# Performance work log

Measured on AMD Instinct MI355X. Metric: run time of the kernel, lower is better.

## Reference

```python
import jax, jax.numpy as jnp
import numpy as np


def setup_inputs() -> dict:
    key = jax.random.key(0)
    ks = jax.random.split(key, 8)
    B, S, A = 128, 256, 128   # rows, seq, channels
    H, KD, VD, O = 8, 16, 16, 128
    w_scale = 1.0 / np.sqrt(A)
    return {
        "q_data": jax.random.normal(ks[0], (B, S, A), jnp.float32),
        "bias": jax.random.normal(ks[1], (B, S, S), jnp.float32),
        "nonbatched_bias": jax.random.normal(ks[2], (S, S), jnp.float32),
        "query_w": jax.random.normal(ks[3], (A, H, KD), jnp.float32) * w_scale,
        "key_w": jax.random.normal(ks[4], (A, H, KD), jnp.float32) * w_scale,
        "value_w": jax.random.normal(ks[5], (A, H, VD), jnp.float32) * w_scale,
        "gating_w": jax.random.normal(ks[6], (A, H, VD), jnp.float32) * w_scale,
        "output_w": jax.random.normal(ks[7], (H, VD, O), jnp.float32) * w_scale,
    }


def reference(q_data, bias, nonbatched_bias, query_w, key_w, value_w, gating_w, output_w):
    # Gated multihead self-attention (AlphaFold grid self-attention).
    key_dim = query_w.shape[-1]
    scale = key_dim ** -0.5
    # fused QKV + gate projections from q_data (self-attention: m_data == q_data)
    q = jnp.einsum('bqa,ahc->bqhc', q_data, query_w) * scale
    k = jnp.einsum('bka,ahc->bkhc', q_data, key_w)
    v = jnp.einsum('bka,ahc->bkhc', q_data, value_w)
    # logits [B, H, Q, K] + batched bias + shared nonbatched bias
    logits = (jnp.einsum('bqhc,bkhc->bhqk', q, k)
              + bias[:, None, :, :]
              + nonbatched_bias[None, None, :, :])
    weights = jax.nn.softmax(logits, axis=-1)
    weighted_avg = jnp.einsum('bhqk,bkhc->bqhc', weights, v)
    gate = jax.nn.sigmoid(jnp.einsum('bqa,ahc->bqhc', q_data, gating_w))
    out = jnp.einsum('bqhc,hco->bqo', gate * weighted_avg, output_w)
    return out
```

## Files before the change

kernel.cpp:

```cpp
#include <hip/hip_runtime.h>
#include <math.h>

#define BB 128
#define SS 256
#define AA 128
#define HH 8
#define CC 16
#define HCC 128
#define OO 128

typedef float f32x4 __attribute__((ext_vector_type(4)));
typedef short s16x4 __attribute__((ext_vector_type(4)));
typedef unsigned short u16x4 __attribute__((ext_vector_type(4)));

__device__ __forceinline__ unsigned bf16_rne(float x) {
    union { float f; unsigned u; } v; v.f = x;
    return (v.u + 0x7fffu + ((v.u >> 16) & 1u)) >> 16;
}
__device__ __forceinline__ unsigned pack_bf16(float lo, float hi) {
    return bf16_rne(lo) | (bf16_rne(hi) << 16);
}

__device__ __forceinline__ void mfma16(f32x4& d, s16x4 a, s16x4 b) {
#if __has_builtin(__builtin_amdgcn_mfma_f32_16x16x16bf16_1k)
    d = __builtin_amdgcn_mfma_f32_16x16x16bf16_1k(a, b, d, 0, 0, 0);
#else
    asm("v_mfma_f32_16x16x16_bf16 %0, %1, %2, %0" : "+v"(d) : "v"(a), "v"(b));
#endif
}

__global__ __launch_bounds__(256) void prep_w_kernel(
    const float* __restrict__ wq, const float* __restrict__ wk,
    const float* __restrict__ wv, const float* __restrict__ wg,
    const float* __restrict__ wo, unsigned short* __restrict__ wt16)
{
    const int j = blockIdx.x >> 4;
    const int t = ((blockIdx.x & 15) << 8) + threadIdx.x;
    const float* W = (j == 0) ? wq : (j == 1) ? wk : (j == 2) ? wv
                   : (j == 3) ? wg : wo;
    const int outch = t >> 5;
    const int a0 = (t & 31) * 4;
    u16x4 v;
    #pragma unroll
    for (int u = 0; u < 4; ++u)
        v[u] = (unsigned short)bf16_rne(W[(size_t)(a0 + u) * 128 + outch]);
    char* dst = (char*)wt16 + (size_t)j * 32768 + outch * 256
              + ((a0 * 2) ^ ((outch & 7) << 5));
    *(u16x4*)dst = v;
}

__global__ __launch_bounds__(256) void qkvg_mfma_kernel(
    const float* __restrict__ qdata, const unsigned short* __restrict__ wt16,
    unsigned short* __restrict__ qb, unsigned short* __restrict__ kb,
    unsigned short* __restrict__ vtb, float* __restrict__ g_ws)
{
    __shared__ char wlds[32768];
    const int tid = threadIdx.x;
    const int w = tid >> 6;
    const int lane = tid & 63;
    const int lo = lane & 15, gg = lane >> 4;
    const int sb = blockIdx.x * 64;
    const int s = sb + w * 16 + lo;
    const int b = sb >> 8;
    const int srow = (sb & 255) + w * 16;

    s16x4 qd[8];
    {
        const float* qp = qdata + (size_t)s * AA;
        #pragma unroll
        for (int t = 0; t < 8; ++t) {
            float4 f = *(const float4*)(qp + t * 16 + gg * 4);
            unsigned w0 = pack_bf16(f.x, f.y), w1 = pack_bf16(f.z, f.w);
            s16x4 q; ((unsigned*)&q)[0] = w0; ((unsigned*)&q)[1] = w1;
            qd[t] = q;
        }
    }

    for (int m = 0; m < 4; ++m) {
        __syncthreads();
        {
            const uint4* src = (const uint4*)((const char*)wt16 + m * 32768);
            uint4* dst = (uint4*)wlds;
            #pragma unroll
            for (int i = 0; i < 8; ++i) dst[i * 256 + tid] = src[i * 256 + tid];
        }
        __syncthreads();

        #pragma unroll
        for (int cf = 0; cf < 8; ++cf) {
            s16x4 wf[8];
            #pragma unroll
            for (int t = 0; t < 8; ++t) {
                int boff = (cf * 16 + lo) * 256 + ((t * 32 + gg * 8) ^ ((lo & 7) << 5));
                wf[t] = *(const s16x4*)(wlds + boff);
            }
            f32x4 acc = {0.f, 0.f, 0.f, 0.f};
            if (m == 2) {
                #pragma unroll
                for (int t = 0; t < 8; ++t) mfma16(acc, qd[t], wf[t]);
                u16x4 o;
                #pragma unroll
                for (int r = 0; r < 4; ++r) o[r] = (unsigned short)bf16_rne(acc[r]);
                *(u16x4*)(vtb + (((size_t)b * HH + cf) * CC + lo) * SS
                          + srow + gg * 4) = o;
            } else {
                #pragma unroll
                for (int t = 0; t < 8; ++t) mfma16(acc, wf[t], qd[t]);
                if (m == 0) {
                    u16x4 o;
                    #pragma unroll
                    for (int r = 0; r < 4; ++r)
                        o[r] = (unsigned short)bf16_rne(acc[r] * 0.25f);
                    *(u16x4*)(qb + (((size_t)b * HH + cf) * SS + srow + lo) * CC
                              + gg * 4) = o;
                } else if (m == 1) {
                    u16x4 o;
                    #pragma unroll
                    for (int r = 0; r < 4; ++r) o[r] = (unsigned short)bf16_rne(acc[r]);
                    *(u16x4*)(kb + (((size_t)b * HH + cf) * SS + srow + lo) * CC
                              + gg * 4) = o;
                } else {
                    float4 g;
                    g.x = 1.f / (1.f + __expf(-acc[0]));
                    g.y = 1.f / (1.f + __expf(-acc[1]));
                    g.z = 1.f / (1.f + __expf(-acc[2]));
                    g.w = 1.f / (1.f + __expf(-acc[3]));
                    *(float4*)(g_ws + ((size_t)b * SS + srow + lo) * HCC
                               + cf * 16 + gg * 4) = g;
                }
            }
        }
    }
}

__global__ __launch_bounds__(512, 2) void attn_mfma_kernel(
    const unsigned short* __restrict__ qb,
    const unsigned short* __restrict__ kb,
    const unsigned short* __restrict__ vtb,
    const float* __restrict__ g_ws,
    const float* __restrict__ bias,
    const float* __restrict__ nb,
    unsigned short* __restrict__ gwa16)
{
    __shared__ float blds[64 * 256];
    const int tid = threadIdx.x;
    const int blk = blockIdx.x;
    const int b = blk >> 2;
    const int Q0 = (blk & 3) * 64;

    {
        const float4* bsrc = (const float4*)(bias + ((size_t)b * SS + Q0) * SS);
        const float4* nsrc = (const float4*)(nb + (size_t)Q0 * SS);
        #pragma unroll
        for (int i = 0; i < 8; ++i) {
            int idx = i * 512 + tid;
            int r = idx >> 6, c4 = idx & 63;
            float4 bv = bsrc[idx];
            float4 nv = nsrc[idx];
            bv.x += nv.x; bv.y += nv.y; bv.z += nv.z; bv.w += nv.w;
            int byteoff = r * 1024 + ((c4 * 16) ^ ((r & 7) << 4));
            *(float4*)((char*)blds + byteoff) = bv;
        }
    }
    __syncthreads();

    const int wv = tid >> 6;
    const int lane = tid & 63;
    const int lo = lane & 15, gg = lane >> 4;
    const size_t bh = (size_t)b * HH + wv;

    s16x4 kf[16], vf[16];
    {
        const unsigned short* kp = kb + bh * SS * CC;
        const unsigned short* vp = vtb + bh * CC * SS;
        #pragma unroll
        for (int t = 0; t < 16; ++t)
            kf[t] = *(const s16x4*)(kp + (t * 16 + lo) * CC + gg * 4);
        #pragma unroll
        for (int t = 0; t < 16; ++t)
            vf[t] = *(const s16x4*)(vp + lo * SS + t * 16 + gg * 4);
    }
    const unsigned short* qp = qb + bh * SS * CC;

    for (int qt = 0; qt < 4; ++qt) {
        const int qrow = Q0 + qt * 16 + lo;
        s16x4 qf = *(const s16x4*)(qp + qrow * CC + gg * 4);
        const int rl = qt * 16 + lo;
        f32x4 S[16];
        #pragma unroll
        for (int t = 0; t < 16; ++t) {
            int byteoff = rl * 1024 + (((t * 4 + gg) * 16) ^ ((rl & 7) << 4));
            S[t] = *(const f32x4*)((const char*)blds + byteoff);
        }
        #pragma unroll
        for (int t = 0; t < 16; ++t) mfma16(S[t], kf[t], qf);
        asm volatile("s_nop 7\n\ts_nop 7");

        float lsum = 0.f;
        unsigned pw[32];
        #pragma unroll
        for (int t = 0; t < 16; ++t) {
            float p0 = __expf(S[t][0] - 12.f), p1 = __expf(S[t][1] - 12.f);
            float p2 = __expf(S[t][2] - 12.f), p3 = __expf(S[t][3] - 12.f);
            lsum += (p0 + p1) + (p2 + p3);
            pw[t * 2]     = pack_bf16(p0, p1);
            pw[t * 2 + 1] = pack_bf16(p2, p3);
        }
        lsum += __shfl_xor(lsum, 16);
        lsum += __shfl_xor(lsum, 32);

        f32x4 W0 = {0.f, 0.f, 0.f, 0.f}, W1 = {0.f, 0.f, 0.f, 0.f};
        asm volatile("s_nop 7");
        #pragma unroll
        for (int t = 0; t < 16; t += 2) {
            s16x4 pa; ((unsigned*)&pa)[0] = pw[t * 2];     ((unsigned*)&pa)[1] = pw[t * 2 + 1];
            mfma16(W0, vf[t], pa);
            s16x4 pb; ((unsigned*)&pb)[0] = pw[t * 2 + 2]; ((unsigned*)&pb)[1] = pw[t * 2 + 3];
            mfma16(W1, vf[t + 1], pb);
        }
        asm volatile("s_nop 7\n\ts_nop 7");

        const float inv = 1.f / lsum;
        const size_t rbase = ((size_t)b * SS + qrow) * HCC + wv * 16 + gg * 4;
        float4 gt = *(const float4*)(g_ws + rbase);
        unsigned w0 = pack_bf16((W0[0] + W1[0]) * inv * gt.x,
                                (W0[1] + W1[1]) * inv * gt.y);
        unsigned w1 = pack_bf16((W0[2] + W1[2]) * inv * gt.z,
                                (W0[3] + W1[3]) * inv * gt.w);
        uint2 st; st.x = w0; st.y = w1;
        *(uint2*)(gwa16 + rbase) = st;
    }
}

__global__ __launch_bounds__(256) void outproj_mfma_kernel(
    const unsigned short* __restrict__ gwa16,
    const unsigned short* __restrict__ wt16o,
    float* __restrict__ out)
{
    __shared__ char wlds[32768];
    const int tid = threadIdx.x;
    const int w = tid >> 6;
    const int lane = tid & 63;
    const int lo = lane & 15, gg = lane >> 4;
    const int sb = blockIdx.x * 64;
    const int s = sb + w * 16 + lo;

    s16x4 gw[8];
    {
        const unsigned short* gp = gwa16 + (size_t)s * HCC;
        #pragma unroll
        for (int t = 0; t < 8; ++t)
            gw[t] = *(const s16x4*)(gp + t * 16 + gg * 4);
    }
    {
        const uint4* src = (const uint4*)wt16o;
        uint4* dst = (uint4*)wlds;
        #pragma unroll
        for (int i = 0; i < 8; ++i) dst[i * 256 + tid] = src[i * 256 + tid];
    }
    __syncthreads();

    #pragma unroll
    for (int cf = 0; cf < 8; ++cf) {
        s16x4 wf[8];
        #pragma unroll
        for (int t = 0; t < 8; ++t) {
            int boff = (cf * 16 + lo) * 256 + ((t * 32 + gg * 8) ^ ((lo & 7) << 5));
            wf[t] = *(const s16x4*)(wlds + boff);
        }
        f32x4 acc = {0.f, 0.f, 0.f, 0.f};
        #pragma unroll
        for (int t = 0; t < 8; ++t) mfma16(acc, wf[t], gw[t]);
        float4 o4; o4.x = acc[0]; o4.y = acc[1]; o4.z = acc[2]; o4.w = acc[3];
        *(float4*)(out + (size_t)s * OO + cf * 16 + gg * 4) = o4;
    }
}

extern "C" void kernel_launch(void* const* d_in, const int* in_sizes, int n_in,
                              void* d_out, int out_size, void* d_ws, size_t ws_size,
                              hipStream_t stream) {
    const float* qdata = (const float*)d_in[0];
    const float* bias  = (const float*)d_in[1];
    const float* nb    = (const float*)d_in[2];
    const float* wq    = (const float*)d_in[3];
    const float* wk    = (const float*)d_in[4];
    const float* wv    = (const float*)d_in[5];
    const float* wg    = (const float*)d_in[6];
    const float* wo    = (const float*)d_in[7];
    float* out = (float*)d_out;

    const size_t QKV = (size_t)BB * HH * SS * CC;
    unsigned short* qb    = (unsigned short*)d_ws;
    unsigned short* kbp   = qb + QKV;
    unsigned short* vtb   = kbp + QKV;
    unsigned short* gwa16 = vtb + QKV;
    unsigned short* wt16  = gwa16 + QKV;
    float* g_ws = (float*)(wt16 + 5 * 16384);

    prep_w_kernel<<<dim3(80), dim3(256), 0, stream>>>(wq, wk, wv, wg, wo, wt16);
    qkvg_mfma_kernel<<<dim3((BB * SS) / 64), dim3(256), 0, stream>>>(
        qdata, wt16, qb, kbp, vtb, g_ws);
    attn_mfma_kernel<<<dim3(BB * 4), dim3(512), 0, stream>>>(
        qb, kbp, vtb, g_ws, bias, nb, gwa16);
    outproj_mfma_kernel<<<dim3((BB * SS) / 64), dim3(256), 0, stream>>>(
        gwa16, wt16 + 4 * 16384, out);
}
```

Before: 161.7 us.

## Fuse output projection into attention kernel and split QKVG projection across grid

The output projection moves into the attention kernel. Gated weighted averages are staged as bf16 in shared memory together with the output weights, which removes the gwa16 round trip through global memory and one kernel launch. The QKVG projection kernel now reads weights directly from global memory (unswizzled layout) instead of staging them in LDS, and its four weight matrices are split across a 2-wide grid Y dimension for more parallelism. Launch bounds are raised for occupancy. The costs are a larger LDS footprint (64KB) in the attention kernel and redundant q_data loads and conversions in the projection kernel.

```diff
diff --git a/kernel.cpp b/kernel.cpp
--- a/kernel.cpp
+++ b/kernel.cpp
@@ -44,17 +44,16 @@
     #pragma unroll
     for (int u = 0; u < 4; ++u)
         v[u] = (unsigned short)bf16_rne(W[(size_t)(a0 + u) * 128 + outch]);
-    char* dst = (char*)wt16 + (size_t)j * 32768 + outch * 256
-              + ((a0 * 2) ^ ((outch & 7) << 5));
-    *(u16x4*)dst = v;
-}
-
-__global__ __launch_bounds__(256) void qkvg_mfma_kernel(
+    int off = a0 * 2;
+    if (j == 4) off ^= (outch & 7) << 5;
+    *(u16x4*)((char*)wt16 + (size_t)j * 32768 + outch * 256 + off) = v;
+}
+
+__global__ __launch_bounds__(256, 4) void qkvg_mfma_kernel(
     const float* __restrict__ qdata, const unsigned short* __restrict__ wt16,
     unsigned short* __restrict__ qb, unsigned short* __restrict__ kb,
     unsigned short* __restrict__ vtb, float* __restrict__ g_ws)
 {
-    __shared__ char wlds[32768];
     const int tid = threadIdx.x;
     const int w = tid >> 6;
     const int lane = tid & 63;
@@ -76,24 +75,15 @@
         }
     }
 
-    for (int m = 0; m < 4; ++m) {
-        __syncthreads();
-        {
-            const uint4* src = (const uint4*)((const char*)wt16 + m * 32768);
-            uint4* dst = (uint4*)wlds;
-            #pragma unroll
-            for (int i = 0; i < 8; ++i) dst[i * 256 + tid] = src[i * 256 + tid];
-        }
-        __syncthreads();
-
+    const int m0 = blockIdx.y * 2;
+    for (int m = m0; m < m0 + 2; ++m) {
+        const unsigned short* wb = wt16 + (size_t)m * 16384;
         #pragma unroll
         for (int cf = 0; cf < 8; ++cf) {
             s16x4 wf[8];
             #pragma unroll
-            for (int t = 0; t < 8; ++t) {
-                int boff = (cf * 16 + lo) * 256 + ((t * 32 + gg * 8) ^ ((lo & 7) << 5));
-                wf[t] = *(const s16x4*)(wlds + boff);
-            }
+            for (int t = 0; t < 8; ++t)
+                wf[t] = *(const s16x4*)(wb + (cf * 16 + lo) * 128 + t * 16 + gg * 4);
             f32x4 acc = {0.f, 0.f, 0.f, 0.f};
             if (m == 2) {
                 #pragma unroll
@@ -133,16 +123,17 @@
     }
 }
 
-__global__ __launch_bounds__(512, 2) void attn_mfma_kernel(
+__global__ __launch_bounds__(512, 4) void attn_fused_kernel(
     const unsigned short* __restrict__ qb,
     const unsigned short* __restrict__ kb,
     const unsigned short* __restrict__ vtb,
     const float* __restrict__ g_ws,
     const float* __restrict__ bias,
     const float* __restrict__ nb,
-    unsigned short* __restrict__ gwa16)
+    const unsigned short* __restrict__ wo16,
+    float* __restrict__ out)
 {
-    __shared__ float blds[64 * 256];
+    __shared__ char smem[65536];
     const int tid = threadIdx.x;
     const int blk = blockIdx.x;
     const int b = blk >> 2;
@@ -159,7 +150,7 @@
             float4 nv = nsrc[idx];
             bv.x += nv.x; bv.y += nv.y; bv.z += nv.z; bv.w += nv.w;
             int byteoff = r * 1024 + ((c4 * 16) ^ ((r & 7) << 4));
-            *(float4*)((char*)blds + byteoff) = bv;
+            *(float4*)(smem + byteoff) = bv;
         }
     }
     __syncthreads();
@@ -182,6 +173,7 @@
     }
     const unsigned short* qp = qb + bh * SS * CC;
 
+    f32x4 ov[4];
     for (int qt = 0; qt < 4; ++qt) {
         const int qrow = Q0 + qt * 16 + lo;
         s16x4 qf = *(const s16x4*)(qp + qrow * CC + gg * 4);
@@ -190,7 +182,7 @@
         #pragma unroll
         for (int t = 0; t < 16; ++t) {
             int byteoff = rl * 1024 + (((t * 4 + gg) * 16) ^ ((rl & 7) << 4));
-            S[t] = *(const f32x4*)((const char*)blds + byteoff);
+            S[t] = *(const f32x4*)(smem + byteoff);
         }
         #pragma unroll
         for (int t = 0; t < 16; ++t) mfma16(S[t], kf[t], qf);
@@ -221,58 +213,55 @@
         asm volatile("s_nop 7\n\ts_nop 7");
 
         const float inv = 1.f / lsum;
-        const size_t rbase = ((size_t)b * SS + qrow) * HCC + wv * 16 + gg * 4;
-        float4 gt = *(const float4*)(g_ws + rbase);
-        unsigned w0 = pack_bf16((W0[0] + W1[0]) * inv * gt.x,
-                                (W0[1] + W1[1]) * inv * gt.y);
-        unsigned w1 = pack_bf16((W0[2] + W1[2]) * inv * gt.z,
-                                (W0[3] + W1[3]) * inv * gt.w);
-        uint2 st; st.x = w0; st.y = w1;
-        *(uint2*)(gwa16 + rbase) = st;
-    }
-}
-
-__global__ __launch_bounds__(256) void outproj_mfma_kernel(
-    const unsigned short* __restrict__ gwa16,
-    const unsigned short* __restrict__ wt16o,
-    float* __restrict__ out)
-{
-    __shared__ char wlds[32768];
-    const int tid = threadIdx.x;
-    const int w = tid >> 6;
-    const int lane = tid & 63;
-    const int lo = lane & 15, gg = lane >> 4;
-    const int sb = blockIdx.x * 64;
-    const int s = sb + w * 16 + lo;
-
-    s16x4 gw[8];
-    {
-        const unsigned short* gp = gwa16 + (size_t)s * HCC;
-        #pragma unroll
-        for (int t = 0; t < 8; ++t)
-            gw[t] = *(const s16x4*)(gp + t * 16 + gg * 4);
-    }
-    {
-        const uint4* src = (const uint4*)wt16o;
-        uint4* dst = (uint4*)wlds;
-        #pragma unroll
-        for (int i = 0; i < 8; ++i) dst[i * 256 + tid] = src[i * 256 + tid];
-    }
+        float4 gt = *(const float4*)(g_ws + ((size_t)b * SS + qrow) * HCC
+                                     + wv * 16 + gg * 4);
+        f32x4 o;
+        o[0] = (W0[0] + W1[0]) * inv * gt.x;
+        o[1] = (W0[1] + W1[1]) * inv * gt.y;
+        o[2] = (W0[2] + W1[2]) * inv * gt.z;
+        o[3] = (W0[3] + W1[3]) * inv * gt.w;
+        ov[qt] = o;
+    }
+
     __syncthreads();
-
-    #pragma unroll
-    for (int cf = 0; cf < 8; ++cf) {
-        s16x4 wf[8];
-        #pragma unroll
-        for (int t = 0; t < 8; ++t) {
-            int boff = (cf * 16 + lo) * 256 + ((t * 32 + gg * 8) ^ ((lo & 7) << 5));
-            wf[t] = *(const s16x4*)(wlds + boff);
-        }
-        f32x4 acc = {0.f, 0.f, 0.f, 0.f};
-        #pragma unroll
-        for (int t = 0; t < 8; ++t) mfma16(acc, wf[t], gw[t]);
-        float4 o4; o4.x = acc[0]; o4.y = acc[1]; o4.z = acc[2]; o4.w = acc[3];
-        *(float4*)(out + (size_t)s * OO + cf * 16 + gg * 4) = o4;
+    {
+        #pragma unroll
+        for (int qt = 0; qt < 4; ++qt) {
+            int rl = qt * 16 + lo;
+            uint2 pk;
+            pk.x = pack_bf16(ov[qt][0], ov[qt][1]);
+            pk.y = pack_bf16(ov[qt][2], ov[qt][3]);
+            int byteoff = rl * 256 + ((wv * 32 + gg * 8) ^ ((rl & 7) << 4));
+            *(uint2*)(smem + byteoff) = pk;
+        }
+        const uint4* src = (const uint4*)wo16;
+        uint4* dst = (uint4*)(smem + 16384);
+        #pragma unroll
+        for (int i = 0; i < 4; ++i) dst[i * 512 + tid] = src[i * 512 + tid];
+    }
+    __syncthreads();
+
+    {
+        const int rt = wv & 3;
+        const int ob = (wv >> 2) * 4;
+        const int r = rt * 16 + lo;
+        const int orow = ((size_t)0, Q0) + rt * 16 + lo;
+        #pragma unroll
+        for (int oi = 0; oi < 4; ++oi) {
+            const int ot = ob + oi;
+            f32x4 acc = {0.f, 0.f, 0.f, 0.f};
+            #pragma unroll
+            for (int kt = 0; kt < 8; ++kt) {
+                s16x4 wf = *(const s16x4*)(smem + 16384 + (ot * 16 + lo) * 256
+                             + ((kt * 32 + gg * 8) ^ ((lo & 7) << 5)));
+                s16x4 gb = *(const s16x4*)(smem + r * 256
+                             + ((kt * 32 + gg * 8) ^ ((r & 7) << 4)));
+                mfma16(acc, wf, gb);
+            }
+            float4 o4; o4.x = acc[0]; o4.y = acc[1]; o4.z = acc[2]; o4.w = acc[3];
+            *(float4*)(out + ((size_t)b * SS + Q0 + rt * 16 + lo) * OO
+                       + ot * 16 + gg * 4) = o4;
+        }
     }
 }
 
@@ -290,18 +279,15 @@
     float* out = (float*)d_out;
 
     const size_t QKV = (size_t)BB * HH * SS * CC;
-    unsigned short* qb    = (unsigned short*)d_ws;
-    unsigned short* kbp   = qb + QKV;
-    unsigned short* vtb   = kbp + QKV;
-    unsigned short* gwa16 = vtb + QKV;
-    unsigned short* wt16  = gwa16 + QKV;
+    unsigned short* qb   = (unsigned short*)d_ws;
+    unsigned short* kbp  = qb + QKV;
+    unsigned short* vtb  = kbp + QKV;
+    unsigned short* wt16 = vtb + QKV;
     float* g_ws = (float*)(wt16 + 5 * 16384);
 
     prep_w_kernel<<<dim3(80), dim3(256), 0, stream>>>(wq, wk, wv, wg, wo, wt16);
-    qkvg_mfma_kernel<<<dim3((BB * SS) / 64), dim3(256), 0, stream>>>(
+    qkvg_mfma_kernel<<<dim3((BB * SS) / 64, 2), dim3(256), 0, stream>>>(
         qdata, wt16, qb, kbp, vtb, g_ws);
-    attn_mfma_kernel<<<dim3(BB * 4), dim3(512), 0, stream>>>(
-        qb, kbp, vtb, g_ws, bias, nb, gwa16);
-    outproj_mfma_kernel<<<dim3((BB * SS) / 64), dim3(256), 0, stream>>>(
-        gwa16, wt16 + 4 * 16384, out);
-}
+    attn_fused_kernel<<<dim3(BB * 4), dim3(512), 0, stream>>>(
+        qb, kbp, vtb, g_ws, bias, nb, wt16 + 4 * 16384, out);
+}
```

Result: slower. 243.3 us (+50.5%).
